# Performance work log

Measured on AMD Instinct MI355X. Metric: run time of the kernel, lower is better.

Reference implementation:

```python
import jax, jax.numpy as jnp
import numpy as np

N_EMBD = 384
BLOCK_SIZE = 256

def setup_inputs() -> dict:
    key = jax.random.key(0)
    k1, k2 = jax.random.split(key)
    B, T = 512, 256
    x = jax.random.normal(k1, (B, T, N_EMBD), dtype=jnp.float32)
    # nn.Linear(384, 192, bias=False): store as [in, out] so projection is x @ w
    w_qkv = jax.random.normal(k2, (N_EMBD, 3 * 64), dtype=jnp.float32) * (1.0 / np.sqrt(N_EMBD))
    return {"x": x, "w_qkv": w_qkv}

def reference(x, w_qkv):
    B, T, C = x.shape  # C == n_embd == 384
    qkv = jnp.einsum('btc,cd->btd', x, w_qkv)       # [B,T,3*hs]
    q, k, v = jnp.split(qkv, 3, axis=-1)            # each [B,T,hs]
    scale = 1.0 / jnp.sqrt(jnp.float32(C))          # NOTE: scales by full embed dim C, per source
    wei = jnp.einsum('btd,bsd->bts', q, k) * scale  # [B,T,T]
    causal = jnp.tril(jnp.ones((T, T), dtype=bool))
    wei = jnp.where(causal, wei, -jnp.inf)
    wei = jax.nn.softmax(wei, axis=-1)
    # dropout is identity in eval mode
    return jnp.einsum('bts,bsd->btd', wei, v)       # [B,T,hs]
```

## Files before the change

### kernel.cpp

```cpp
#include <hip/hip_runtime.h>
#include <hip/hip_bf16.h>


constexpr int B  = 512;
constexpr int T  = 256;
constexpr int C  = 384;
constexpr int HS = 64;
constexpr long BT = (long)B * T;
constexpr long PLANE = BT * HS;
constexpr float SCALE = 0.05103103630798288f;

constexpr int NT   = 192;
constexpr int MT   = 128;
constexpr int BK   = 64;
constexpr int ROWP = 72;
constexpr int VP   = 264;

typedef _Float16 f16x8 __attribute__((ext_vector_type(8)));
typedef _Float16 f16x4 __attribute__((ext_vector_type(4)));
typedef __fp16   fp16x2_raw __attribute__((ext_vector_type(2)));
typedef float    f32x4 __attribute__((ext_vector_type(4)));

__global__ __launch_bounds__(256)
void wt_kernel(const float* __restrict__ w, _Float16* __restrict__ wt) {
    const int idx = blockIdx.x * 256 + threadIdx.x;
    if (idx < NT * C) {
        const int n = idx / C, k = idx % C;
        wt[idx] = (_Float16)w[k * NT + n];
    }
}

__global__ __launch_bounds__(256)
void proj_kernel(const float* __restrict__ x, const _Float16* __restrict__ wt,
                 _Float16* __restrict__ qp, _Float16* __restrict__ kp,
                 _Float16* __restrict__ vtp) {
    __shared__ __align__(16) _Float16 XL[MT * ROWP];
    __shared__ __align__(16) _Float16 WL[NT * ROWP];

    const int tid  = threadIdx.x;
    const int lane = tid & 63;
    const int wv   = tid >> 6;
    const int wm   = wv >> 1, wn = wv & 1;
    const int l15  = lane & 15, quad = lane >> 4;
    const long row0 = (long)blockIdx.x * MT;

    f32x4 acc[4][6];
#pragma unroll
    for (int mi = 0; mi < 4; ++mi)
#pragma unroll
        for (int ni = 0; ni < 6; ++ni) acc[mi][ni] = (f32x4)0.f;

    float4 xr[8];
#pragma unroll
    for (int i = 0; i < 8; ++i) {
        const int flat = tid + 256 * i;
        const int r = flat >> 4, seg = flat & 15;
        xr[i] = *(const float4*)(x + (row0 + r) * C + seg * 4);
    }

    for (int kc = 0; kc < C / BK; ++kc) {
        const int k0 = kc * BK;
        uint4 wr[6];
#pragma unroll
        for (int i = 0; i < 6; ++i) {
            const int flat = tid + 256 * i;
            const int n = flat >> 3, seg = flat & 7;
            wr[i] = *(const uint4*)(wt + n * C + k0 + seg * 8);
        }
        __syncthreads();
#pragma unroll
        for (int i = 0; i < 8; ++i) {
            const int flat = tid + 256 * i;
            const int r = flat >> 4, seg = flat & 15;
            union { fp16x2_raw h[2]; uint2 u; } cv;
            cv.h[0] = __builtin_amdgcn_cvt_pkrtz(xr[i].x, xr[i].y);
            cv.h[1] = __builtin_amdgcn_cvt_pkrtz(xr[i].z, xr[i].w);
            *(uint2*)&XL[r * ROWP + seg * 4] = cv.u;
        }
#pragma unroll
        for (int i = 0; i < 6; ++i) {
            const int flat = tid + 256 * i;
            const int n = flat >> 3, seg = flat & 7;
            *(uint4*)&WL[n * ROWP + seg * 8] = wr[i];
        }
        if (kc < C / BK - 1) {
#pragma unroll
            for (int i = 0; i < 8; ++i) {
                const int flat = tid + 256 * i;
                const int r = flat >> 4, seg = flat & 15;
                xr[i] = *(const float4*)(x + (row0 + r) * C + k0 + BK + seg * 4);
            }
        }
        __syncthreads();

#pragma unroll
        for (int s = 0; s < 2; ++s) {
            const int kk = s * 32 + quad * 8;
            f16x8 a[4], bfr[6];
#pragma unroll
            for (int mi = 0; mi < 4; ++mi)
                a[mi] = *(const f16x8*)&XL[(wm * 64 + mi * 16 + l15) * ROWP + kk];
#pragma unroll
            for (int ni = 0; ni < 6; ++ni)
                bfr[ni] = *(const f16x8*)&WL[(wn * 96 + ni * 16 + l15) * ROWP + kk];
#pragma unroll
            for (int mi = 0; mi < 4; ++mi)
#pragma unroll
                for (int ni = 0; ni < 6; ++ni)
                    acc[mi][ni] = __builtin_amdgcn_mfma_f32_16x16x32_f16(
                        a[mi], bfr[ni], acc[mi][ni], 0, 0, 0);
        }
    }

#pragma unroll
    for (int mi = 0; mi < 4; ++mi) {
        const long grow0 = row0 + wm * 64 + mi * 16 + quad * 4;
        const int bb = (int)(grow0 >> 8);
        const int t0 = (int)(grow0 & 255);
#pragma unroll
        for (int ni = 0; ni < 6; ++ni) {
            const int colbase = wn * 96 + ni * 16;
            const int col = colbase + l15;
            if (colbase < 64) {
#pragma unroll
                for (int r = 0; r < 4; ++r)
                    qp[(grow0 + r) * HS + col] = (_Float16)acc[mi][ni][r];
            } else if (colbase < 128) {
#pragma unroll
                for (int r = 0; r < 4; ++r)
                    kp[(grow0 + r) * HS + (col - 64)] = (_Float16)acc[mi][ni][r];
            } else {
                f16x4 pv;
#pragma unroll
                for (int r = 0; r < 4; ++r) pv[r] = (_Float16)acc[mi][ni][r];
                *(f16x4*)&vtp[(long)bb * (HS * T) + (col - 128) * T + t0] = pv;
            }
        }
    }
}

__global__ __launch_bounds__(512)
void attn_kernel(const _Float16* __restrict__ qp, const _Float16* __restrict__ kp,
                 const _Float16* __restrict__ vtp, float* __restrict__ out) {
    __shared__ __align__(16) _Float16 VL[HS * VP];

    const int b = blockIdx.x, tid = threadIdx.x;
    const int lane = tid & 63, wv = tid >> 6;
    const int l15 = lane & 15, quad = lane >> 4;

    const _Float16* Vg = vtp + (long)b * (HS * T);
#pragma unroll
    for (int i = 0; i < 4; ++i) {
        const int flat = tid + 512 * i;
        const int r = flat >> 5, seg = flat & 31;
        *(uint4*)&VL[r * VP + seg * 8] = *(const uint4*)(Vg + r * T + seg * 8);
    }
    __syncthreads();

    const int s0 = wv, s1 = 15 - wv;
    const _Float16* Qg = qp + (long)b * T * HS;
    const _Float16* Kg = kp + (long)b * T * HS;

    f16x8 qf0[2], qf1[2];
#pragma unroll
    for (int ks = 0; ks < 2; ++ks) {
        qf0[ks] = *(const f16x8*)(Qg + (s0 * 16 + l15) * HS + ks * 32 + quad * 8);
        qf1[ks] = *(const f16x8*)(Qg + (s1 * 16 + l15) * HS + ks * 32 + quad * 8);
    }

    f32x4 o0[4], o1[4];
#pragma unroll
    for (int di = 0; di < 4; ++di) { o0[di] = (f32x4)0.f; o1[di] = (f32x4)0.f; }
    float lp0 = 0.f, lp1 = 0.f;

    for (int kt = 0; kt <= s1; ++kt) {
        const int key0 = kt * 16;
        const f16x8 ka0 = *(const f16x8*)(Kg + (key0 + l15) * HS + quad * 8);
        const f16x8 ka1 = *(const f16x8*)(Kg + (key0 + l15) * HS + 32 + quad * 8);
        f16x4 va[4];
#pragma unroll
        for (int di = 0; di < 4; ++di)
            va[di] = *(const f16x4*)&VL[(di * 16 + l15) * VP + key0 + quad * 4];

        {
            f32x4 s = {0.f, 0.f, 0.f, 0.f};
            s = __builtin_amdgcn_mfma_f32_16x16x32_f16(ka0, qf1[0], s, 0, 0, 0);
            s = __builtin_amdgcn_mfma_f32_16x16x32_f16(ka1, qf1[1], s, 0, 0, 0);
            const bool dm = (kt == s1);
            f16x4 pb; float ps = 0.f;
#pragma unroll
            for (int r = 0; r < 4; ++r) {
                float pr = __expf(s[r] * SCALE);
                pr = (dm && (quad * 4 + r > l15)) ? 0.f : pr;
                ps += pr; pb[r] = (_Float16)pr;
            }
            lp1 += ps;
#pragma unroll
            for (int di = 0; di < 4; ++di)
                o1[di] = __builtin_amdgcn_mfma_f32_16x16x16f16(va[di], pb, o1[di], 0, 0, 0);
        }
        if (kt <= s0) {
            f32x4 s = {0.f, 0.f, 0.f, 0.f};
            s = __builtin_amdgcn_mfma_f32_16x16x32_f16(ka0, qf0[0], s, 0, 0, 0);
            s = __builtin_amdgcn_mfma_f32_16x16x32_f16(ka1, qf0[1], s, 0, 0, 0);
            const bool dm = (kt == s0);
            f16x4 pb; float ps = 0.f;
#pragma unroll
            for (int r = 0; r < 4; ++r) {
                float pr = __expf(s[r] * SCALE);
                pr = (dm && (quad * 4 + r > l15)) ? 0.f : pr;
                ps += pr; pb[r] = (_Float16)pr;
            }
            lp0 += ps;
#pragma unroll
            for (int di = 0; di < 4; ++di)
                o0[di] = __builtin_amdgcn_mfma_f32_16x16x16f16(va[di], pb, o0[di], 0, 0, 0);
        }
    }

    lp0 += __shfl_xor(lp0, 16, 64); lp0 += __shfl_xor(lp0, 32, 64);
    lp1 += __shfl_xor(lp1, 16, 64); lp1 += __shfl_xor(lp1, 32, 64);
    const float i0 = 1.0f / lp0, i1 = 1.0f / lp1;

    float* ob = out + (long)b * T * HS;
#pragma unroll
    for (int di = 0; di < 4; ++di) {
        float4 v0, v1;
        v0.x = o0[di][0] * i0; v0.y = o0[di][1] * i0;
        v0.z = o0[di][2] * i0; v0.w = o0[di][3] * i0;
        v1.x = o1[di][0] * i1; v1.y = o1[di][1] * i1;
        v1.z = o1[di][2] * i1; v1.w = o1[di][3] * i1;
        *(float4*)&ob[(s0 * 16 + l15) * HS + di * 16 + quad * 4] = v0;
        *(float4*)&ob[(s1 * 16 + l15) * HS + di * 16 + quad * 4] = v1;
    }
}

extern "C" void kernel_launch(void* const* d_in, const int* in_sizes, int n_in,
                              void* d_out, int out_size, void* d_ws, size_t ws_size,
                              hipStream_t stream) {
    const float* x = (const float*)d_in[0];
    const float* w = (const float*)d_in[1];
    float* out = (float*)d_out;

    _Float16* qp  = (_Float16*)d_ws;
    _Float16* kp  = qp + PLANE;
    _Float16* vtp = kp + PLANE;
    _Float16* wt  = vtp + PLANE;

    wt_kernel<<<dim3((NT * C + 255) / 256), dim3(256), 0, stream>>>(w, wt);
    proj_kernel<<<dim3((unsigned)(BT / MT)), dim3(256), 0, stream>>>(x, wt, qp, kp, vtp);
    attn_kernel<<<dim3(B), dim3(512), 0, stream>>>(qp, kp, vtp, out);
}
```

Baseline: 333.1 us.

## Drop LDS staging; load MFMA fragments from global and prefetch K/V

The projection kernel no longer stages x and W tiles through shared memory with barriers. Each wave now loads its MFMA fragments straight from global memory, converting x to fp16 in registers. The attention kernel drops the V shared-memory copy and its barrier, reads V fragments from global, and register-prefetches the next K/V tile one iteration ahead. This removes LDS traffic and synchronisation, but the projection kernel now issues many small strided global loads, and the two wave columns (wn) each re-read the same x rows, which relies on the cache for reuse.

```diff
diff --git a/kernel.cpp b/kernel.cpp
--- a/kernel.cpp
+++ b/kernel.cpp
@@ -10,11 +10,9 @@
 constexpr long PLANE = BT * HS;
 constexpr float SCALE = 0.05103103630798288f;
 
-constexpr int NT   = 192;
-constexpr int MT   = 128;
-constexpr int BK   = 64;
-constexpr int ROWP = 72;
-constexpr int VP   = 264;
+constexpr int NT = 192;
+constexpr int MT = 128;
+constexpr int BK = 64;
 
 typedef _Float16 f16x8 __attribute__((ext_vector_type(8)));
 typedef _Float16 f16x4 __attribute__((ext_vector_type(4)));
@@ -34,9 +32,6 @@
 void proj_kernel(const float* __restrict__ x, const _Float16* __restrict__ wt,
                  _Float16* __restrict__ qp, _Float16* __restrict__ kp,
                  _Float16* __restrict__ vtp) {
-    __shared__ __align__(16) _Float16 XL[MT * ROWP];
-    __shared__ __align__(16) _Float16 WL[NT * ROWP];
-
     const int tid  = threadIdx.x;
     const int lane = tid & 63;
     const int wv   = tid >> 6;
@@ -44,72 +39,47 @@
     const int l15  = lane & 15, quad = lane >> 4;
     const long row0 = (long)blockIdx.x * MT;
 
+    const float*    xb = x  + (row0 + wm * 64 + l15) * C + quad * 8;
+    const _Float16* wb = wt + (wn * 96 + l15) * C + quad * 8;
+
     f32x4 acc[4][6];
 #pragma unroll
     for (int mi = 0; mi < 4; ++mi)
 #pragma unroll
         for (int ni = 0; ni < 6; ++ni) acc[mi][ni] = (f32x4)0.f;
-
-    float4 xr[8];
-#pragma unroll
-    for (int i = 0; i < 8; ++i) {
-        const int flat = tid + 256 * i;
-        const int r = flat >> 4, seg = flat & 15;
-        xr[i] = *(const float4*)(x + (row0 + r) * C + seg * 4);
-    }
 
     for (int kc = 0; kc < C / BK; ++kc) {
         const int k0 = kc * BK;
-        uint4 wr[6];
-#pragma unroll
-        for (int i = 0; i < 6; ++i) {
-            const int flat = tid + 256 * i;
-            const int n = flat >> 3, seg = flat & 7;
-            wr[i] = *(const uint4*)(wt + n * C + k0 + seg * 8);
-        }
-        __syncthreads();
-#pragma unroll
-        for (int i = 0; i < 8; ++i) {
-            const int flat = tid + 256 * i;
-            const int r = flat >> 4, seg = flat & 15;
-            union { fp16x2_raw h[2]; uint2 u; } cv;
-            cv.h[0] = __builtin_amdgcn_cvt_pkrtz(xr[i].x, xr[i].y);
-            cv.h[1] = __builtin_amdgcn_cvt_pkrtz(xr[i].z, xr[i].w);
-            *(uint2*)&XL[r * ROWP + seg * 4] = cv.u;
-        }
-#pragma unroll
-        for (int i = 0; i < 6; ++i) {
-            const int flat = tid + 256 * i;
-            const int n = flat >> 3, seg = flat & 7;
-            *(uint4*)&WL[n * ROWP + seg * 8] = wr[i];
-        }
-        if (kc < C / BK - 1) {
-#pragma unroll
-            for (int i = 0; i < 8; ++i) {
-                const int flat = tid + 256 * i;
-                const int r = flat >> 4, seg = flat & 15;
-                xr[i] = *(const float4*)(x + (row0 + r) * C + k0 + BK + seg * 4);
-            }
-        }
-        __syncthreads();
-
-#pragma unroll
-        for (int s = 0; s < 2; ++s) {
-            const int kk = s * 32 + quad * 8;
-            f16x8 a[4], bfr[6];
-#pragma unroll
-            for (int mi = 0; mi < 4; ++mi)
-                a[mi] = *(const f16x8*)&XL[(wm * 64 + mi * 16 + l15) * ROWP + kk];
-#pragma unroll
-            for (int ni = 0; ni < 6; ++ni)
-                bfr[ni] = *(const f16x8*)&WL[(wn * 96 + ni * 16 + l15) * ROWP + kk];
+        f16x8 af[4][2];
+#pragma unroll
+        for (int mi = 0; mi < 4; ++mi)
+#pragma unroll
+            for (int s = 0; s < 2; ++s) {
+                const float* p = xb + (long)(mi * 16) * C + k0 + s * 32;
+                const f32x4 lo = *(const f32x4*)p;
+                const f32x4 hi = *(const f32x4*)(p + 4);
+                union { fp16x2_raw h[4]; f16x8 v; } u;
+                u.h[0] = __builtin_amdgcn_cvt_pkrtz(lo[0], lo[1]);
+                u.h[1] = __builtin_amdgcn_cvt_pkrtz(lo[2], lo[3]);
+                u.h[2] = __builtin_amdgcn_cvt_pkrtz(hi[0], hi[1]);
+                u.h[3] = __builtin_amdgcn_cvt_pkrtz(hi[2], hi[3]);
+                af[mi][s] = u.v;
+            }
+        f16x8 bf[6][2];
+#pragma unroll
+        for (int ni = 0; ni < 6; ++ni)
+#pragma unroll
+            for (int s = 0; s < 2; ++s)
+                bf[ni][s] = *(const f16x8*)(wb + (long)(ni * 16) * C + k0 + s * 32);
+
+#pragma unroll
+        for (int s = 0; s < 2; ++s)
 #pragma unroll
             for (int mi = 0; mi < 4; ++mi)
 #pragma unroll
                 for (int ni = 0; ni < 6; ++ni)
                     acc[mi][ni] = __builtin_amdgcn_mfma_f32_16x16x32_f16(
-                        a[mi], bfr[ni], acc[mi][ni], 0, 0, 0);
-        }
+                        af[mi][s], bf[ni][s], acc[mi][ni], 0, 0, 0);
     }
 
 #pragma unroll
@@ -142,24 +112,14 @@
 __global__ __launch_bounds__(512)
 void attn_kernel(const _Float16* __restrict__ qp, const _Float16* __restrict__ kp,
                  const _Float16* __restrict__ vtp, float* __restrict__ out) {
-    __shared__ __align__(16) _Float16 VL[HS * VP];
-
     const int b = blockIdx.x, tid = threadIdx.x;
     const int lane = tid & 63, wv = tid >> 6;
     const int l15 = lane & 15, quad = lane >> 4;
 
+    const int s0 = wv, s1 = 15 - wv;
+    const _Float16* Qg = qp  + (long)b * T * HS;
+    const _Float16* Kg = kp  + (long)b * T * HS;
     const _Float16* Vg = vtp + (long)b * (HS * T);
-#pragma unroll
-    for (int i = 0; i < 4; ++i) {
-        const int flat = tid + 512 * i;
-        const int r = flat >> 5, seg = flat & 31;
-        *(uint4*)&VL[r * VP + seg * 8] = *(const uint4*)(Vg + r * T + seg * 8);
-    }
-    __syncthreads();
-
-    const int s0 = wv, s1 = 15 - wv;
-    const _Float16* Qg = qp + (long)b * T * HS;
-    const _Float16* Kg = kp + (long)b * T * HS;
 
     f16x8 qf0[2], qf1[2];
 #pragma unroll
@@ -173,14 +133,22 @@
     for (int di = 0; di < 4; ++di) { o0[di] = (f32x4)0.f; o1[di] = (f32x4)0.f; }
     float lp0 = 0.f, lp1 = 0.f;
 
+    f16x8 ka0 = *(const f16x8*)(Kg + l15 * HS + quad * 8);
+    f16x8 ka1 = *(const f16x8*)(Kg + l15 * HS + 32 + quad * 8);
+    f16x4 va[4];
+#pragma unroll
+    for (int di = 0; di < 4; ++di)
+        va[di] = *(const f16x4*)(Vg + (di * 16 + l15) * T + quad * 4);
+
     for (int kt = 0; kt <= s1; ++kt) {
-        const int key0 = kt * 16;
-        const f16x8 ka0 = *(const f16x8*)(Kg + (key0 + l15) * HS + quad * 8);
-        const f16x8 ka1 = *(const f16x8*)(Kg + (key0 + l15) * HS + 32 + quad * 8);
-        f16x4 va[4];
+        const int ktn = (kt < s1) ? kt + 1 : kt;
+        const int keyn = ktn * 16;
+        f16x8 nk0 = *(const f16x8*)(Kg + (keyn + l15) * HS + quad * 8);
+        f16x8 nk1 = *(const f16x8*)(Kg + (keyn + l15) * HS + 32 + quad * 8);
+        f16x4 nva[4];
 #pragma unroll
         for (int di = 0; di < 4; ++di)
-            va[di] = *(const f16x4*)&VL[(di * 16 + l15) * VP + key0 + quad * 4];
+            nva[di] = *(const f16x4*)(Vg + (di * 16 + l15) * T + keyn + quad * 4);
 
         {
             f32x4 s = {0.f, 0.f, 0.f, 0.f};
@@ -216,6 +184,10 @@
             for (int di = 0; di < 4; ++di)
                 o0[di] = __builtin_amdgcn_mfma_f32_16x16x16f16(va[di], pb, o0[di], 0, 0, 0);
         }
+
+        ka0 = nk0; ka1 = nk1;
+#pragma unroll
+        for (int di = 0; di < 4; ++di) va[di] = nva[di];
     }
 
     lp0 += __shfl_xor(lp0, 16, 64); lp0 += __shfl_xor(lp0, 32, 64);
```

Result: slower. 397.4 us (+19.3%).
